# Kernel tuning notes

Hardware: AMD Instinct MI355X
Metric: run time of the kernel (lower is better)

## Reference

```python
import jax, jax.numpy as jnp
import numpy as np

H, W = 512, 512          # resized_height, resized_width
R = 2                    # cdist norm order
B, NGT = 4, 64
MAX_DIST = float(np.sqrt(H ** 2 + W ** 2))
EPS = 1e-6


def setup_inputs() -> dict:
    key = jax.random.key(0)
    k1, k2, k3, k4 = jax.random.split(key, 4)
    prob_map = jax.random.uniform(k1, (B, H, W), dtype=jnp.float32)
    # all entries > 0.2 so the torch filter prob_y[prob_y>0.2] keeps every point
    prob_y = 0.2 + 0.79 * jax.random.uniform(k2, (B, NGT), dtype=jnp.float32)
    gt = jax.random.uniform(k3, (B, NGT, 2), dtype=jnp.float32) * jnp.array([H - 1, W - 1], jnp.float32)
    orig_sizes = jax.random.randint(k4, (B, 2), 512, 2048, dtype=jnp.int32)
    return {"prob_map": prob_map, "prob_y": prob_y, "gt": gt, "orig_sizes": orig_sizes}


def _pixel_locations():
    # cartesian([arange(H), arange(W)]) -> (H*W, 2), row-major
    ii, jj = jnp.meshgrid(jnp.arange(H), jnp.arange(W), indexing="ij")
    return jnp.stack([ii, jj], axis=-1).reshape(-1, 2).astype(jnp.float32)


def _ghd(prob_map, prob_y, gt, orig_sizes):
    locs = _pixel_locations()                      # (P, 2), P = H*W
    resized = jnp.array([H, W], jnp.float32)

    def per_batch(pm, py, g, osz):
        nf = osz.astype(jnp.float32) / resized     # (2,) norm factor
        nx = nf * locs                             # (P, 2)
        ny = nf * g                                # (G, 2)
        diff = jnp.abs(nx[:, None, :] - ny[None, :, :])   # (P, G, 2)
        d = jnp.sum(diff ** R, axis=-1) ** (1.0 / R)      # (P, G)
        p = pm.reshape(-1)                         # (P,)
        n_est_pts = jnp.sum(p)
        n_gt_sum = jnp.sum(jnp.where(py > 0.2, py, 0.0))
        weighted = p[:, None] * py[None, :] * d    # p_x * p_y * d
        term_1 = jnp.sum(jnp.min(weighted, axis=1)) / (n_est_pts + EPS)
        dense = (1.0 - p[:, None]) * MAX_DIST + weighted
        term_2 = jnp.sum(jnp.min(dense, axis=0)) / (n_gt_sum + EPS)
        return term_1, term_2

    t1, t2 = jax.vmap(per_batch)(prob_map, prob_y, gt, orig_sizes)
    return t1.mean() + t2.mean()


def reference(prob_map, prob_y, gt, orig_sizes):
    return _ghd(prob_map, prob_y, gt, orig_sizes)
```

## Files before the change

kernel.cpp:

```cpp
#include <hip/hip_runtime.h>
#include <math.h>

#define HH 512
#define WW 512
#define PP (HH * WW)
#define GG 64
#define BB 4
#define THREADS 512
#define TILE 1024
#define NT (PP / TILE)
#define MAX_DIST 724.0773439350246f
#define EPSV 1e-6f
#define BIGF 3.4e38f


__launch_bounds__(THREADS, 8)
__global__ void ghd_main(const float* __restrict__ prob_map,
                         const float* __restrict__ prob_y,
                         const float* __restrict__ gt,
                         const int*   __restrict__ osz,
                         float*       __restrict__ ws) {
    const int t    = blockIdx.x;
    const int b    = blockIdx.y;
    const int tid  = threadIdx.x;
    const int lane = tid & 63;
    const int wave = tid >> 6;

    __shared__ float4 gdat[GG];
    __shared__ __align__(16) float sp[TILE];
    __shared__ float  wmin[8][GG];
    __shared__ float  s_t1[8], s_ne[8];

    const float nf0 = (float)osz[2 * b]     * (1.0f / HH);
    const float nf1 = (float)osz[2 * b + 1] * (1.0f / WW);

    if (tid < GG) {
        float py = prob_y[b * GG + tid];
        gdat[tid] = make_float4(nf0 * gt[(b * GG + tid) * 2],
                                nf1 * gt[(b * GG + tid) * 2 + 1],
                                py, py * py);
    }
    ((float2*)sp)[tid] = ((const float2*)(prob_map + (size_t)b * PP + t * TILE))[tid];
    __syncthreads();

    const int   pid0 = t * TILE + tid * 2;
    const float p0 = sp[tid * 2], p1 = sp[tid * 2 + 1];
    const float nx0  = nf0 * (float)(pid0 >> 9);
    const float nx1a = nf1 * (float)(pid0 & (WW - 1));
    float ma = BIGF, mb = BIGF;
#pragma unroll 16
    for (int g = 0; g < GG; ++g) {
        float4 gd  = gdat[g];
        float  dx  = nx0 - gd.x;
        float  dx2 = dx * dx;
        float  da  = nx1a - gd.y;
        float  db  = da + nf1;
        ma = fminf(ma, gd.w * fmaf(da, da, dx2));
        mb = fminf(mb, gd.w * fmaf(db, db, dx2));
    }
    float t1 = p0 * __builtin_amdgcn_sqrtf(ma) + p1 * __builtin_amdgcn_sqrtf(mb);
    float ne = p0 + p1;

    const float4 gme  = gdat[lane];
    const int    s0   = wave * (TILE / 8);
    const int    pidw = t * TILE + s0;
    const float  dxw  = nf0 * (float)(pidw >> 9) - gme.x;
    const float  dx2w = dxw * dxw;
    const float  mgy  = -gme.y;
    float jf  = (float)(pidw & (WW - 1));
    float gm0 = BIGF, gm1 = BIGF;
    const float4* __restrict__ sp4 = (const float4*)(sp + s0);
#pragma unroll 8
    for (int k = 0; k < TILE / 8 / 4; ++k) {
        float4 q = sp4[k];
        float dy0 = fmaf(nf1, jf,        mgy);
        float dy1 = fmaf(nf1, jf + 1.0f, mgy);
        float dy2 = fmaf(nf1, jf + 2.0f, mgy);
        float dy3 = fmaf(nf1, jf + 3.0f, mgy);
        float e0 = __builtin_amdgcn_sqrtf(fmaf(dy0, dy0, dx2w));
        float e1 = __builtin_amdgcn_sqrtf(fmaf(dy1, dy1, dx2w));
        float e2 = __builtin_amdgcn_sqrtf(fmaf(dy2, dy2, dx2w));
        float e3 = __builtin_amdgcn_sqrtf(fmaf(dy3, dy3, dx2w));
        gm0 = fminf(gm0, fmaf(q.x * gme.z, e0, fmaf(-q.x, MAX_DIST, MAX_DIST)));
        gm1 = fminf(gm1, fmaf(q.y * gme.z, e1, fmaf(-q.y, MAX_DIST, MAX_DIST)));
        gm0 = fminf(gm0, fmaf(q.z * gme.z, e2, fmaf(-q.z, MAX_DIST, MAX_DIST)));
        gm1 = fminf(gm1, fmaf(q.w * gme.z, e3, fmaf(-q.w, MAX_DIST, MAX_DIST)));
        jf += 4.0f;
    }
    wmin[wave][lane] = fminf(gm0, gm1);

#pragma unroll
    for (int off = 1; off < 64; off <<= 1) {
        t1 += __shfl_xor(t1, off);
        ne += __shfl_xor(ne, off);
    }
    if (lane == 0) { s_t1[wave] = t1; s_ne[wave] = ne; }
    __syncthreads();

    if (tid == 0) {
        float st = 0.0f, sn = 0.0f;
#pragma unroll
        for (int w = 0; w < 8; ++w) { st += s_t1[w]; sn += s_ne[w]; }
        ws[256  + b * NT + t] = st;
        ws[1280 + b * NT + t] = sn;
    }
    if (tid < GG) {
        float v = wmin[0][tid];
#pragma unroll
        for (int w = 1; w < 8; ++w) v = fminf(v, wmin[w][tid]);
        atomicMin(reinterpret_cast<unsigned*>(ws) + b * GG + tid, __float_as_uint(v));
    }
}

__global__ void ghd_final(const float* __restrict__ prob_y,
                          const float* __restrict__ ws,
                          float*       __restrict__ out) {
    const int tid = threadIdx.x;
    const int b = tid >> 6;
    const int g = tid & 63;

    float mv  = __uint_as_float(reinterpret_cast<const unsigned*>(ws)[b * GG + g]);
    float py  = prob_y[b * GG + g];
    float pyf = (py > 0.2f) ? py : 0.0f;

    float4 tv = ((const float4*)(ws + 256))[b * (NT / 4) + g];
    float4 nv = ((const float4*)(ws + 1280))[b * (NT / 4) + g];
    float t1s = tv.x + tv.y + tv.z + tv.w;
    float nes = nv.x + nv.y + nv.z + nv.w;

#pragma unroll
    for (int off = 1; off < 64; off <<= 1) {
        mv  += __shfl_xor(mv, off);
        pyf += __shfl_xor(pyf, off);
        t1s += __shfl_xor(t1s, off);
        nes += __shfl_xor(nes, off);
    }
    __shared__ float res[4];
    if (g == 0) res[b] = t1s / (nes + EPSV) + mv / (pyf + EPSV);
    __syncthreads();
    if (tid == 0) out[0] = 0.25f * (res[0] + res[1] + res[2] + res[3]);
}

extern "C" void kernel_launch(void* const* d_in, const int* in_sizes, int n_in,
                              void* d_out, int out_size, void* d_ws, size_t ws_size,
                              hipStream_t stream) {
    const float* prob_map = (const float*)d_in[0];
    const float* prob_y   = (const float*)d_in[1];
    const float* gt       = (const float*)d_in[2];
    const int*   osz      = (const int*)d_in[3];
    float* out = (float*)d_out;
    float* ws  = (float*)d_ws;

    hipMemsetAsync(ws, 0x7f, BB * GG * sizeof(unsigned), stream);

    dim3 grid(NT, BB);
    ghd_main<<<grid, THREADS, 0, stream>>>(prob_map, prob_y, gt, osz, ws);
    ghd_final<<<1, 256, 0, stream>>>(prob_y, ws, out);
}
```

Baseline: 86.44 us.

## Broadcast GT and prob values via readlane instead of LDS staging

Drops the LDS staging of ground-truth coordinates and the prob-map tile, along with the first __syncthreads. Each wave now loads its own 128-pixel segment and the 64 GT points straight into registers and broadcasts them across lanes with readlane, so both inner loops read scalar operands instead of LDS. Both loops are fully unrolled. The cost is extra scalar readlane instructions and more code, and wave-level loading may change how well the global loads coalesce.

```diff
diff --git a/kernel.cpp b/kernel.cpp
--- a/kernel.cpp
+++ b/kernel.cpp
@@ -14,6 +14,10 @@
 #define BIGF 3.4e38f
 
 
+__device__ __forceinline__ float rdlane(float v, int l) {
+    return __int_as_float(__builtin_amdgcn_readlane(__float_as_int(v), l));
+}
+
 __launch_bounds__(THREADS, 8)
 __global__ void ghd_main(const float* __restrict__ prob_map,
                          const float* __restrict__ prob_y,
@@ -26,66 +30,54 @@
     const int lane = tid & 63;
     const int wave = tid >> 6;
 
-    __shared__ float4 gdat[GG];
-    __shared__ __align__(16) float sp[TILE];
-    __shared__ float  wmin[8][GG];
-    __shared__ float  s_t1[8], s_ne[8];
+    __shared__ float wmin[8][GG];
+    __shared__ float s_t1[8], s_ne[8];
 
     const float nf0 = (float)osz[2 * b]     * (1.0f / HH);
     const float nf1 = (float)osz[2 * b + 1] * (1.0f / WW);
 
-    if (tid < GG) {
-        float py = prob_y[b * GG + tid];
-        gdat[tid] = make_float4(nf0 * gt[(b * GG + tid) * 2],
-                                nf1 * gt[(b * GG + tid) * 2 + 1],
-                                py, py * py);
+    const float2 gxy = ((const float2*)gt)[b * GG + lane];
+    const float  gx  = nf0 * gxy.x;
+    const float  gy  = nf1 * gxy.y;
+    const float  py  = prob_y[b * GG + lane];
+    const float  pyq = py * py;
+
+    const int    seg0 = t * TILE + wave * 128;
+    const float2 p2   = ((const float2*)(prob_map + (size_t)b * PP + seg0))[lane];
+    const int    pid0 = seg0 + 2 * lane;
+    const float  nx0  = nf0 * (float)(pid0 >> 9);
+    const float  nx1a = nf1 * (float)(pid0 & (WW - 1));
+
+    float ma = BIGF, mb = BIGF;
+#pragma unroll
+    for (int g = 0; g < GG; ++g) {
+        float sgx = rdlane(gx,  g);
+        float sgy = rdlane(gy,  g);
+        float sw  = rdlane(pyq, g);
+        float dx  = nx0 - sgx;
+        float dx2 = dx * dx;
+        float da  = nx1a - sgy;
+        float db  = da + nf1;
+        ma = fminf(ma, sw * fmaf(da, da, dx2));
+        mb = fminf(mb, sw * fmaf(db, db, dx2));
     }
-    ((float2*)sp)[tid] = ((const float2*)(prob_map + (size_t)b * PP + t * TILE))[tid];
-    __syncthreads();
+    float t1 = p2.x * __builtin_amdgcn_sqrtf(ma) + p2.y * __builtin_amdgcn_sqrtf(mb);
+    float ne = p2.x + p2.y;
 
-    const int   pid0 = t * TILE + tid * 2;
-    const float p0 = sp[tid * 2], p1 = sp[tid * 2 + 1];
-    const float nx0  = nf0 * (float)(pid0 >> 9);
-    const float nx1a = nf1 * (float)(pid0 & (WW - 1));
-    float ma = BIGF, mb = BIGF;
-#pragma unroll 16
-    for (int g = 0; g < GG; ++g) {
-        float4 gd  = gdat[g];
-        float  dx  = nx0 - gd.x;
-        float  dx2 = dx * dx;
-        float  da  = nx1a - gd.y;
-        float  db  = da + nf1;
-        ma = fminf(ma, gd.w * fmaf(da, da, dx2));
-        mb = fminf(mb, gd.w * fmaf(db, db, dx2));
-    }
-    float t1 = p0 * __builtin_amdgcn_sqrtf(ma) + p1 * __builtin_amdgcn_sqrtf(mb);
-    float ne = p0 + p1;
-
-    const float4 gme  = gdat[lane];
-    const int    s0   = wave * (TILE / 8);
-    const int    pidw = t * TILE + s0;
-    const float  dxw  = nf0 * (float)(pidw >> 9) - gme.x;
-    const float  dx2w = dxw * dxw;
-    const float  mgy  = -gme.y;
-    float jf  = (float)(pidw & (WW - 1));
+    const float dxw  = nf0 * (float)(seg0 >> 9) - gx;
+    const float dx2w = dxw * dxw;
+    const float ny0  = nf1 * (float)(seg0 & (WW - 1)) - gy;
     float gm0 = BIGF, gm1 = BIGF;
-    const float4* __restrict__ sp4 = (const float4*)(sp + s0);
-#pragma unroll 8
-    for (int k = 0; k < TILE / 8 / 4; ++k) {
-        float4 q = sp4[k];
-        float dy0 = fmaf(nf1, jf,        mgy);
-        float dy1 = fmaf(nf1, jf + 1.0f, mgy);
-        float dy2 = fmaf(nf1, jf + 2.0f, mgy);
-        float dy3 = fmaf(nf1, jf + 3.0f, mgy);
-        float e0 = __builtin_amdgcn_sqrtf(fmaf(dy0, dy0, dx2w));
-        float e1 = __builtin_amdgcn_sqrtf(fmaf(dy1, dy1, dx2w));
-        float e2 = __builtin_amdgcn_sqrtf(fmaf(dy2, dy2, dx2w));
-        float e3 = __builtin_amdgcn_sqrtf(fmaf(dy3, dy3, dx2w));
-        gm0 = fminf(gm0, fmaf(q.x * gme.z, e0, fmaf(-q.x, MAX_DIST, MAX_DIST)));
-        gm1 = fminf(gm1, fmaf(q.y * gme.z, e1, fmaf(-q.y, MAX_DIST, MAX_DIST)));
-        gm0 = fminf(gm0, fmaf(q.z * gme.z, e2, fmaf(-q.z, MAX_DIST, MAX_DIST)));
-        gm1 = fminf(gm1, fmaf(q.w * gme.z, e3, fmaf(-q.w, MAX_DIST, MAX_DIST)));
-        jf += 4.0f;
+#pragma unroll
+    for (int k = 0; k < 64; ++k) {
+        float pa  = rdlane(p2.x, k);
+        float pb  = rdlane(p2.y, k);
+        float dya = fmaf((float)(2 * k),     nf1, ny0);
+        float dyb = fmaf((float)(2 * k + 1), nf1, ny0);
+        float ea  = __builtin_amdgcn_sqrtf(fmaf(dya, dya, dx2w));
+        float eb  = __builtin_amdgcn_sqrtf(fmaf(dyb, dyb, dx2w));
+        gm0 = fminf(gm0, fmaf(pa * py, ea, fmaf(-pa, MAX_DIST, MAX_DIST)));
+        gm1 = fminf(gm1, fmaf(pb * py, eb, fmaf(-pb, MAX_DIST, MAX_DIST)));
     }
     wmin[wave][lane] = fminf(gm0, gm1);
 
```

Result: slower. 92.04 us (+6.5%).
